# Performance work log

Measured on AMD Instinct MI355X. Metric: run time of the kernel, lower is better.

The kernel has to match this reference:

```python
import jax, jax.numpy as jnp
import numpy as np

B, N, D, E = 4, 100000, 128, 262144
HID, OUT, EXTRA = 128, 128, 1


def setup_inputs() -> dict:
    key = jax.random.key(0)
    k1, k2, k3, k4, k5 = jax.random.split(key, 5)
    node_emb = jax.random.normal(k1, (B, N, D), dtype=jnp.float32)
    edge_index = jax.random.randint(k2, (B, E, 2), 0, N, dtype=jnp.int64)
    edge_sel = jax.random.uniform(k3, (B, E, EXTRA), dtype=jnp.float32)
    W1 = jax.random.normal(k4, (2 * D + EXTRA, HID), dtype=jnp.float32) * (1.0 / np.sqrt(2 * D + EXTRA))
    b1 = jnp.zeros((HID,), dtype=jnp.float32)
    W2 = jax.random.normal(k5, (HID, OUT), dtype=jnp.float32) * (1.0 / np.sqrt(HID))
    b2 = jnp.zeros((OUT,), dtype=jnp.float32)
    return {"node_emb": node_emb, "edge_index": edge_index, "edge_sel": edge_sel,
            "W1": W1, "b1": b1, "W2": W2, "b2": b2}


def reference(node_emb, edge_index, edge_sel, W1, b1, W2, b2):
    n = node_emb.shape[1]
    idx_u = jnp.clip(edge_index[..., 0], 0, n - 1)  # [B,E]
    idx_v = jnp.clip(edge_index[..., 1], 0, n - 1)  # [B,E]
    batch = jnp.arange(node_emb.shape[0])[:, None]  # [B,1]
    u = node_emb[batch, idx_u]  # [B,E,D]
    v = node_emb[batch, idx_v]  # [B,E,D]
    x = jnp.concatenate([u, v, edge_sel.astype(jnp.float32)], axis=-1)  # [B,E,2D+1]
    h = jax.nn.relu(jnp.einsum('bef,fh->beh', x, W1) + b1)
    return jax.nn.relu(jnp.einsum('beh,ho->beo', h, W2) + b2)
```

## Files before the change

### kernel.cpp

```cpp
#include <hip/hip_runtime.h>
#include <stdint.h>

#define BB 4
#define NN 100000
#define DD 128
#define EE 262144
#define HH 128
#define OO 128

typedef __attribute__((ext_vector_type(4))) float f32x4;
typedef __attribute__((ext_vector_type(8))) __bf16 bf16x8;

static __device__ __forceinline__ unsigned short f2bf(float f) {
    union { float f; unsigned u; } v; v.f = f;
    return (unsigned short)((v.u + 0x7fffu + ((v.u >> 16) & 1u)) >> 16);
}

__global__ __launch_bounds__(256) void prep_w1(const float* __restrict__ W1,
                                               unsigned short* __restrict__ w1f) {
    int t = blockIdx.x * 256 + threadIdx.x;
    if (t >= 256 * 128) return;
    int k = t >> 7, n = t & 127;
    int kt = k >> 5, quad = (k >> 3) & 3, j = k & 7;
    int nt = n >> 4, nl = n & 15;
    int f = ((((kt * 8 + nt) * 64) + quad * 16 + nl) << 3) | j;
    w1f[f] = f2bf(W1[t]);
}

__global__ __launch_bounds__(256, 2) void edge_mlp(
    const float* __restrict__ node_emb,
    const int* __restrict__ edge_index,
    const float* __restrict__ edge_sel,
    const float* __restrict__ W1,
    const float* __restrict__ b1,
    const float* __restrict__ W2,
    const float* __restrict__ b2,
    const unsigned short* __restrict__ w1f,
    float* __restrict__ out)
{
    __shared__ unsigned short w2f[16384];
    __shared__ unsigned short hst[4][16 * 136];

    const int tid = threadIdx.x;

    for (int s = tid; s < 16384; s += 256) {
        int k = s >> 7, n = s & 127;
        int f = ((((k >> 5) * 8 + (n >> 4)) * 64) + ((k >> 3) & 3) * 16 + (n & 15)) * 8 + (k & 7);
        w2f[f] = f2bf(W2[s]);
    }
    __syncthreads();

    const int lane = tid & 63;
    const int wv = tid >> 6;
    const int nl = lane & 15;
    const int quad = lane >> 4;

    float b1v[8], w1cv[8], b2v[8];
#pragma unroll
    for (int nt = 0; nt < 8; ++nt) {
        b1v[nt] = b1[nt * 16 + nl];
        w1cv[nt] = W1[256 * 128 + nt * 16 + nl];
        b2v[nt] = b2[nt * 16 + nl];
    }

    const int eb = blockIdx.x * 256 + wv * 64;
    const int bat = eb >> 18;
    const size_t nbase = (size_t)bat * NN * DD;

    unsigned ou[4], ov[4];
#pragma unroll
    for (int mt = 0; mt < 4; ++mt) {
        int e = eb + mt * 16 + nl;
        int iu = edge_index[(size_t)e * 2 + 0];
        int iv = edge_index[(size_t)e * 2 + 1];
        iu = min(max(iu, 0), NN - 1);
        iv = min(max(iv, 0), NN - 1);
        ou[mt] = (unsigned)nbase + (unsigned)iu * DD + quad * 8;
        ov[mt] = (unsigned)nbase + (unsigned)iv * DD + quad * 8;
    }

    f32x4 acc[4][8];
#pragma unroll
    for (int mt = 0; mt < 4; ++mt)
#pragma unroll
        for (int nt = 0; nt < 8; ++nt)
            acc[mt][nt] = f32x4{0.f, 0.f, 0.f, 0.f};

    const bf16x8* wbase = (const bf16x8*)w1f;
#pragma unroll
    for (int kt = 0; kt < 8; ++kt) {
        bf16x8 af[4];
#pragma unroll
        for (int mt = 0; mt < 4; ++mt) {
            unsigned o = ((kt < 4) ? ou[mt] : ov[mt]) + (kt & 3) * 32;
            f32x4 x0 = *(const f32x4*)(node_emb + o);
            f32x4 x1 = *(const f32x4*)(node_emb + o + 4);
            bf16x8 a;
            a[0] = (__bf16)x0[0]; a[1] = (__bf16)x0[1];
            a[2] = (__bf16)x0[2]; a[3] = (__bf16)x0[3];
            a[4] = (__bf16)x1[0]; a[5] = (__bf16)x1[1];
            a[6] = (__bf16)x1[2]; a[7] = (__bf16)x1[3];
            af[mt] = a;
        }
#pragma unroll
        for (int nt = 0; nt < 8; ++nt) {
            bf16x8 bf = wbase[(kt * 8 + nt) * 64 + lane];
#pragma unroll
            for (int mt = 0; mt < 4; ++mt)
                acc[mt][nt] = __builtin_amdgcn_mfma_f32_16x16x32_bf16(af[mt], bf, acc[mt][nt], 0, 0, 0);
        }
    }

    const bf16x8* w2base = (const bf16x8*)w2f;
    unsigned short* hw = hst[wv];

#pragma unroll
    for (int pr = 0; pr < 2; ++pr) {
        bf16x8 ha[2][4];
#pragma unroll
        for (int q = 0; q < 2; ++q) {
            const int mt = pr * 2 + q;
            float sel[4];
#pragma unroll
            for (int i = 0; i < 4; ++i)
                sel[i] = edge_sel[(size_t)(eb + mt * 16 + quad * 4 + i)];
#pragma unroll
            for (int nt = 0; nt < 8; ++nt) {
#pragma unroll
                for (int i = 0; i < 4; ++i) {
                    float hv = acc[mt][nt][i] + sel[i] * w1cv[nt] + b1v[nt];
                    hv = fmaxf(hv, 0.f);
                    hw[(quad * 4 + i) * 136 + nt * 16 + nl] = f2bf(hv);
                }
            }
            __syncthreads();
#pragma unroll
            for (int kt2 = 0; kt2 < 4; ++kt2)
                ha[q][kt2] = *(const bf16x8*)(hw + nl * 136 + kt2 * 32 + quad * 8);
            __syncthreads();
        }

        f32x4 a2[2][8];
#pragma unroll
        for (int q = 0; q < 2; ++q)
#pragma unroll
            for (int nt = 0; nt < 8; ++nt)
                a2[q][nt] = f32x4{0.f, 0.f, 0.f, 0.f};

#pragma unroll
        for (int kt2 = 0; kt2 < 4; ++kt2) {
#pragma unroll
            for (int nt = 0; nt < 8; ++nt) {
                bf16x8 bf = w2base[(kt2 * 8 + nt) * 64 + lane];
                a2[0][nt] = __builtin_amdgcn_mfma_f32_16x16x32_bf16(ha[0][kt2], bf, a2[0][nt], 0, 0, 0);
                a2[1][nt] = __builtin_amdgcn_mfma_f32_16x16x32_bf16(ha[1][kt2], bf, a2[1][nt], 0, 0, 0);
            }
        }

#pragma unroll
        for (int q = 0; q < 2; ++q) {
            const int mt = pr * 2 + q;
#pragma unroll
            for (int nt = 0; nt < 8; ++nt) {
#pragma unroll
                for (int i = 0; i < 4; ++i) {
                    float o = a2[q][nt][i] + b2v[nt];
                    o = fmaxf(o, 0.f);
                    out[(size_t)(eb + mt * 16 + quad * 4 + i) * OO + nt * 16 + nl] = o;
                }
            }
        }
    }
}

extern "C" void kernel_launch(void* const* d_in, const int* in_sizes, int n_in,
                              void* d_out, int out_size, void* d_ws, size_t ws_size,
                              hipStream_t stream) {
    const float* node_emb  = (const float*)d_in[0];
    const int*   edge_index= (const int*)d_in[1];
    const float* edge_sel  = (const float*)d_in[2];
    const float* W1        = (const float*)d_in[3];
    const float* b1        = (const float*)d_in[4];
    const float* W2        = (const float*)d_in[5];
    const float* b2        = (const float*)d_in[6];
    unsigned short* w1f    = (unsigned short*)d_ws;
    float* out             = (float*)d_out;

    prep_w1<<<dim3(128), dim3(256), 0, stream>>>(W1, w1f);
    edge_mlp<<<dim3(4096), dim3(256), 0, stream>>>(node_emb, edge_index, edge_sel,
                                                   W1, b1, W2, b2, w1f, out);
}
```

Baseline: 929.8 us.

## Pre-convert node embeddings to bf16, move W2 prep to global, halve tile per block

Adds a prep pass that converts all node embeddings to bf16 in workspace, so the gather reads half the bytes per edge, and a prep kernel that stores W2 pre-swizzled in global memory instead of rebuilding it in LDS every block. Each wave now handles 32 edges instead of 64, with a higher occupancy bound and fewer syncthreads, and outputs are written with nontemporal stores. The bf16 conversion pass reads and writes the whole embedding table (about 205MB read, 102MB write) every call, which may cost more than the gather saves, since only about 2M random rows are gathered. Fallback paths keep the old behaviour when the workspace is too small.

Result: no change. 940.2 us (+1.1%).

```diff
diff --git a/kernel.cpp b/kernel.cpp
--- a/kernel.cpp
+++ b/kernel.cpp
@@ -10,6 +10,7 @@
 
 typedef __attribute__((ext_vector_type(4))) float f32x4;
 typedef __attribute__((ext_vector_type(8))) __bf16 bf16x8;
+typedef __attribute__((ext_vector_type(8))) unsigned short u16x8;
 
 static __device__ __forceinline__ unsigned short f2bf(float f) {
     union { float f; unsigned u; } v; v.f = f;
@@ -19,16 +20,34 @@
 __global__ __launch_bounds__(256) void prep_w1(const float* __restrict__ W1,
                                                unsigned short* __restrict__ w1f) {
     int t = blockIdx.x * 256 + threadIdx.x;
-    if (t >= 256 * 128) return;
     int k = t >> 7, n = t & 127;
-    int kt = k >> 5, quad = (k >> 3) & 3, j = k & 7;
-    int nt = n >> 4, nl = n & 15;
-    int f = ((((kt * 8 + nt) * 64) + quad * 16 + nl) << 3) | j;
+    int f = ((((k >> 5) * 8 + (n >> 4)) * 64) + ((k >> 3) & 3) * 16 + (n & 15)) * 8 + (k & 7);
     w1f[f] = f2bf(W1[t]);
 }
 
-__global__ __launch_bounds__(256, 2) void edge_mlp(
+__global__ __launch_bounds__(256) void prep_w2(const float* __restrict__ W2,
+                                               unsigned short* __restrict__ w2f) {
+    int t = blockIdx.x * 256 + threadIdx.x;
+    int k = t >> 7, n = t & 127;
+    int f = ((((k >> 5) * 8 + (n >> 4)) * 64) + ((k >> 3) & 3) * 16 + (n & 15)) * 8 + (k & 7);
+    w2f[f] = f2bf(W2[t]);
+}
+
+__global__ __launch_bounds__(256) void prep_node(const float* __restrict__ ne,
+                                                 unsigned short* __restrict__ nb) {
+    size_t t = (size_t)blockIdx.x * 256 + threadIdx.x;
+    const f32x4* s = (const f32x4*)ne + (t << 1);
+    f32x4 a = s[0], b = s[1];
+    u16x8 o;
+    o[0] = f2bf(a[0]); o[1] = f2bf(a[1]); o[2] = f2bf(a[2]); o[3] = f2bf(a[3]);
+    o[4] = f2bf(b[0]); o[5] = f2bf(b[1]); o[6] = f2bf(b[2]); o[7] = f2bf(b[3]);
+    *((u16x8*)nb + t) = o;
+}
+
+template<bool BF16N, bool W2LDS>
+__global__ __launch_bounds__(256, 4) void edge_mlp(
     const float* __restrict__ node_emb,
+    const unsigned short* __restrict__ node_bf,
     const int* __restrict__ edge_index,
     const float* __restrict__ edge_sel,
     const float* __restrict__ W1,
@@ -36,138 +55,144 @@
     const float* __restrict__ W2,
     const float* __restrict__ b2,
     const unsigned short* __restrict__ w1f,
+    const unsigned short* __restrict__ w2f,
     float* __restrict__ out)
 {
-    __shared__ unsigned short w2f[16384];
-    __shared__ unsigned short hst[4][16 * 136];
+    __shared__ unsigned short hst[4][2][16 * 136];
+    __shared__ unsigned short w2s[W2LDS ? 16384 : 1];
 
     const int tid = threadIdx.x;
 
-    for (int s = tid; s < 16384; s += 256) {
-        int k = s >> 7, n = s & 127;
-        int f = ((((k >> 5) * 8 + (n >> 4)) * 64) + ((k >> 3) & 3) * 16 + (n & 15)) * 8 + (k & 7);
-        w2f[f] = f2bf(W2[s]);
-    }
-    __syncthreads();
+    if constexpr (W2LDS) {
+        for (int s = tid; s < 16384; s += 256) {
+            int k = s >> 7, n = s & 127;
+            int f = ((((k >> 5) * 8 + (n >> 4)) * 64) + ((k >> 3) & 3) * 16 + (n & 15)) * 8 + (k & 7);
+            w2s[f] = f2bf(W2[s]);
+        }
+        __syncthreads();
+    }
 
     const int lane = tid & 63;
     const int wv = tid >> 6;
     const int nl = lane & 15;
     const int quad = lane >> 4;
 
-    float b1v[8], w1cv[8], b2v[8];
+    float b1v[8], w1cv[8];
 #pragma unroll
     for (int nt = 0; nt < 8; ++nt) {
         b1v[nt] = b1[nt * 16 + nl];
         w1cv[nt] = W1[256 * 128 + nt * 16 + nl];
-        b2v[nt] = b2[nt * 16 + nl];
-    }
-
-    const int eb = blockIdx.x * 256 + wv * 64;
+    }
+
+    const int eb = blockIdx.x * 128 + wv * 32;
     const int bat = eb >> 18;
-    const size_t nbase = (size_t)bat * NN * DD;
-
-    unsigned ou[4], ov[4];
-#pragma unroll
-    for (int mt = 0; mt < 4; ++mt) {
+    const unsigned nbase = (unsigned)bat * (NN * DD);
+
+    unsigned ou[2], ov[2];
+#pragma unroll
+    for (int mt = 0; mt < 2; ++mt) {
         int e = eb + mt * 16 + nl;
         int iu = edge_index[(size_t)e * 2 + 0];
         int iv = edge_index[(size_t)e * 2 + 1];
         iu = min(max(iu, 0), NN - 1);
         iv = min(max(iv, 0), NN - 1);
-        ou[mt] = (unsigned)nbase + (unsigned)iu * DD + quad * 8;
-        ov[mt] = (unsigned)nbase + (unsigned)iv * DD + quad * 8;
-    }
-
-    f32x4 acc[4][8];
-#pragma unroll
-    for (int mt = 0; mt < 4; ++mt)
+        ou[mt] = nbase + (unsigned)iu * DD + quad * 8;
+        ov[mt] = nbase + (unsigned)iv * DD + quad * 8;
+    }
+
+    f32x4 acc[2][8];
+#pragma unroll
+    for (int mt = 0; mt < 2; ++mt)
 #pragma unroll
         for (int nt = 0; nt < 8; ++nt)
             acc[mt][nt] = f32x4{0.f, 0.f, 0.f, 0.f};
 
-    const bf16x8* wbase = (const bf16x8*)w1f;
+    const bf16x8* w1b = (const bf16x8*)w1f;
 #pragma unroll
     for (int kt = 0; kt < 8; ++kt) {
-        bf16x8 af[4];
-#pragma unroll
-        for (int mt = 0; mt < 4; ++mt) {
+        bf16x8 af[2];
+#pragma unroll
+        for (int mt = 0; mt < 2; ++mt) {
             unsigned o = ((kt < 4) ? ou[mt] : ov[mt]) + (kt & 3) * 32;
-            f32x4 x0 = *(const f32x4*)(node_emb + o);
-            f32x4 x1 = *(const f32x4*)(node_emb + o + 4);
-            bf16x8 a;
-            a[0] = (__bf16)x0[0]; a[1] = (__bf16)x0[1];
-            a[2] = (__bf16)x0[2]; a[3] = (__bf16)x0[3];
-            a[4] = (__bf16)x1[0]; a[5] = (__bf16)x1[1];
-            a[6] = (__bf16)x1[2]; a[7] = (__bf16)x1[3];
-            af[mt] = a;
-        }
-#pragma unroll
-        for (int nt = 0; nt < 8; ++nt) {
-            bf16x8 bf = wbase[(kt * 8 + nt) * 64 + lane];
-#pragma unroll
-            for (int mt = 0; mt < 4; ++mt)
-                acc[mt][nt] = __builtin_amdgcn_mfma_f32_16x16x32_bf16(af[mt], bf, acc[mt][nt], 0, 0, 0);
-        }
-    }
-
-    const bf16x8* w2base = (const bf16x8*)w2f;
-    unsigned short* hw = hst[wv];
-
-#pragma unroll
-    for (int pr = 0; pr < 2; ++pr) {
-        bf16x8 ha[2][4];
-#pragma unroll
-        for (int q = 0; q < 2; ++q) {
-            const int mt = pr * 2 + q;
-            float sel[4];
-#pragma unroll
-            for (int i = 0; i < 4; ++i)
-                sel[i] = edge_sel[(size_t)(eb + mt * 16 + quad * 4 + i)];
-#pragma unroll
-            for (int nt = 0; nt < 8; ++nt) {
-#pragma unroll
-                for (int i = 0; i < 4; ++i) {
-                    float hv = acc[mt][nt][i] + sel[i] * w1cv[nt] + b1v[nt];
-                    hv = fmaxf(hv, 0.f);
-                    hw[(quad * 4 + i) * 136 + nt * 16 + nl] = f2bf(hv);
-                }
+            if constexpr (BF16N) {
+                af[mt] = *(const bf16x8*)(node_bf + o);
+            } else {
+                f32x4 x0 = *(const f32x4*)(node_emb + o);
+                f32x4 x1 = *(const f32x4*)(node_emb + o + 4);
+                bf16x8 a;
+                a[0] = (__bf16)x0[0]; a[1] = (__bf16)x0[1];
+                a[2] = (__bf16)x0[2]; a[3] = (__bf16)x0[3];
+                a[4] = (__bf16)x1[0]; a[5] = (__bf16)x1[1];
+                a[6] = (__bf16)x1[2]; a[7] = (__bf16)x1[3];
+                af[mt] = a;
             }
-            __syncthreads();
-#pragma unroll
-            for (int kt2 = 0; kt2 < 4; ++kt2)
-                ha[q][kt2] = *(const bf16x8*)(hw + nl * 136 + kt2 * 32 + quad * 8);
-            __syncthreads();
-        }
-
-        f32x4 a2[2][8];
-#pragma unroll
-        for (int q = 0; q < 2; ++q)
-#pragma unroll
-            for (int nt = 0; nt < 8; ++nt)
-                a2[q][nt] = f32x4{0.f, 0.f, 0.f, 0.f};
-
-#pragma unroll
-        for (int kt2 = 0; kt2 < 4; ++kt2) {
-#pragma unroll
-            for (int nt = 0; nt < 8; ++nt) {
-                bf16x8 bf = w2base[(kt2 * 8 + nt) * 64 + lane];
-                a2[0][nt] = __builtin_amdgcn_mfma_f32_16x16x32_bf16(ha[0][kt2], bf, a2[0][nt], 0, 0, 0);
-                a2[1][nt] = __builtin_amdgcn_mfma_f32_16x16x32_bf16(ha[1][kt2], bf, a2[1][nt], 0, 0, 0);
+        }
+#pragma unroll
+        for (int nt = 0; nt < 8; ++nt) {
+            bf16x8 bf = w1b[(kt * 8 + nt) * 64 + lane];
+            acc[0][nt] = __builtin_amdgcn_mfma_f32_16x16x32_bf16(af[0], bf, acc[0][nt], 0, 0, 0);
+            acc[1][nt] = __builtin_amdgcn_mfma_f32_16x16x32_bf16(af[1], bf, acc[1][nt], 0, 0, 0);
+        }
+    }
+
+#pragma unroll
+    for (int q = 0; q < 2; ++q) {
+        float sel[4];
+#pragma unroll
+        for (int i = 0; i < 4; ++i)
+            sel[i] = edge_sel[(size_t)(eb + q * 16 + quad * 4 + i)];
+        unsigned short* hw = hst[wv][q];
+#pragma unroll
+        for (int nt = 0; nt < 8; ++nt) {
+#pragma unroll
+            for (int i = 0; i < 4; ++i) {
+                float hv = acc[q][nt][i] + sel[i] * w1cv[nt] + b1v[nt];
+                hv = fmaxf(hv, 0.f);
+                hw[(quad * 4 + i) * 136 + nt * 16 + nl] = f2bf(hv);
             }
         }
-
-#pragma unroll
-        for (int q = 0; q < 2; ++q) {
-            const int mt = pr * 2 + q;
-#pragma unroll
-            for (int nt = 0; nt < 8; ++nt) {
-#pragma unroll
-                for (int i = 0; i < 4; ++i) {
-                    float o = a2[q][nt][i] + b2v[nt];
-                    o = fmaxf(o, 0.f);
-                    out[(size_t)(eb + mt * 16 + quad * 4 + i) * OO + nt * 16 + nl] = o;
-                }
+    }
+
+    bf16x8 ha[2][4];
+#pragma unroll
+    for (int q = 0; q < 2; ++q)
+#pragma unroll
+        for (int kt2 = 0; kt2 < 4; ++kt2)
+            ha[q][kt2] = *(const bf16x8*)(hst[wv][q] + nl * 136 + kt2 * 32 + quad * 8);
+
+    f32x4 a2[2][8];
+#pragma unroll
+    for (int q = 0; q < 2; ++q)
+#pragma unroll
+        for (int nt = 0; nt < 8; ++nt)
+            a2[q][nt] = f32x4{0.f, 0.f, 0.f, 0.f};
+
+    const bf16x8* w2b = (const bf16x8*)(W2LDS ? (const unsigned short*)w2s : w2f);
+#pragma unroll
+    for (int kt2 = 0; kt2 < 4; ++kt2) {
+#pragma unroll
+        for (int nt = 0; nt < 8; ++nt) {
+            bf16x8 bf = w2b[(kt2 * 8 + nt) * 64 + lane];
+            a2[0][nt] = __builtin_amdgcn_mfma_f32_16x16x32_bf16(ha[0][kt2], bf, a2[0][nt], 0, 0, 0);
+            a2[1][nt] = __builtin_amdgcn_mfma_f32_16x16x32_bf16(ha[1][kt2], bf, a2[1][nt], 0, 0, 0);
+        }
+    }
+
+    float b2v[8];
+#pragma unroll
+    for (int nt = 0; nt < 8; ++nt)
+        b2v[nt] = b2[nt * 16 + nl];
+
+#pragma unroll
+    for (int q = 0; q < 2; ++q) {
+#pragma unroll
+        for (int nt = 0; nt < 8; ++nt) {
+#pragma unroll
+            for (int i = 0; i < 4; ++i) {
+                float o = a2[q][nt][i] + b2v[nt];
+                o = fmaxf(o, 0.f);
+                __builtin_nontemporal_store(
+                    o, &out[(size_t)(eb + q * 16 + quad * 4 + i) * OO + nt * 16 + nl]);
             }
         }
     }
@@ -183,10 +208,29 @@
     const float* b1        = (const float*)d_in[4];
     const float* W2        = (const float*)d_in[5];
     const float* b2        = (const float*)d_in[6];
-    unsigned short* w1f    = (unsigned short*)d_ws;
     float* out             = (float*)d_out;
 
+    unsigned short* w1f = (unsigned short*)d_ws;
+    const size_t NODE_BYTES = (size_t)BB * NN * DD * 2;
+    const size_t NEED_B = 65536 + 32768;
+    const size_t NEED_A = NEED_B + NODE_BYTES;
+
     prep_w1<<<dim3(128), dim3(256), 0, stream>>>(W1, w1f);
-    edge_mlp<<<dim3(4096), dim3(256), 0, stream>>>(node_emb, edge_index, edge_sel,
-                                                   W1, b1, W2, b2, w1f, out);
-}
+
+    if (ws_size >= NEED_A) {
+        unsigned short* w2f = w1f + 32768;
+        unsigned short* nbf = w2f + 16384;
+        prep_w2<<<dim3(64), dim3(256), 0, stream>>>(W2, w2f);
+        prep_node<<<dim3(25000), dim3(256), 0, stream>>>(node_emb, nbf);
+        edge_mlp<true, false><<<dim3(8192), dim3(256), 0, stream>>>(
+            node_emb, nbf, edge_index, edge_sel, W1, b1, W2, b2, w1f, w2f, out);
+    } else if (ws_size >= NEED_B) {
+        unsigned short* w2f = w1f + 32768;
+        prep_w2<<<dim3(64), dim3(256), 0, stream>>>(W2, w2f);
+        edge_mlp<false, false><<<dim3(8192), dim3(256), 0, stream>>>(
+            node_emb, nullptr, edge_index, edge_sel, W1, b1, W2, b2, w1f, w2f, out);
+    } else {
+        edge_mlp<false, true><<<dim3(8192), dim3(256), 0, stream>>>(
+            node_emb, nullptr, edge_index, edge_sel, W1, b1, W2, b2, w1f, nullptr, out);
+    }
+}
```
